# Kernel tuning notes

Measured on AMD Instinct MI355X. Metric: run time of the kernel, lower is better.

Reference implementation:

```python
import jax, jax.numpy as jnp
import numpy as np

FS, STRIDE, PAD = 3, 1, 1

def setup_inputs() -> dict:
    key = jax.random.key(0)
    k1, k2, k3 = jax.random.split(key, 3)
    N, C, H, W = 4, 256, 64, 64
    out_C = 256
    x = jax.random.normal(k1, (N, C, H, W), jnp.float32)
    # offset/mask conv params (original inits to 0 -> degenerate; use small random)
    offset_w = jax.random.normal(k2, (FS * FS * 3, C, FS, FS), jnp.float32) * 0.01
    offset_b = jnp.zeros((FS * FS * 3,), jnp.float32)
    # xavier_normal-like scale for dcn weight
    dcn_w = jax.random.normal(k3, (out_C, C, FS, FS), jnp.float32) * (1.0 / np.sqrt(C * FS * FS))
    return {"x": x, "offset_w": offset_w, "offset_b": offset_b, "dcn_w": dcn_w}

def _dcnv2(x, offset_w, offset_b, dcn_w):
    fs, stride, pad = FS, STRIDE, PAD
    N, C, H, W = x.shape
    out_C = dcn_w.shape[0]
    K2 = fs * fs
    om = jax.lax.conv_general_dilated(
        x, offset_w, (stride, stride), [(pad, pad), (pad, pad)],
        dimension_numbers=("NCHW", "OIHW", "NCHW")) + offset_b[None, :, None, None]
    Ho, Wo = om.shape[2], om.shape[3]
    offset = om[:, : 2 * K2].reshape(N, K2, 2, Ho, Wo)
    off_y, off_x = offset[:, :, 0], offset[:, :, 1]            # [N,K2,Ho,Wo]
    mask = jax.nn.sigmoid(om[:, 2 * K2:])                      # [N,K2,Ho,Wo]
    # base sampling grid: ori + kernel tap offset
    ky, kx = jnp.meshgrid(jnp.arange(fs), jnp.arange(fs), indexing="ij")
    ky = ky.reshape(K2).astype(jnp.float32)
    kx = kx.reshape(K2).astype(jnp.float32)
    base_y = (jnp.arange(Ho, dtype=jnp.float32) * stride - pad)[None, :, None] + ky[:, None, None]
    base_x = (jnp.arange(Wo, dtype=jnp.float32) * stride - pad)[None, None, :] + kx[:, None, None]
    h_im = base_y[None] + off_y                                # [N,K2,Ho,Wo]
    w_im = base_x[None] + off_x
    y0 = jnp.floor(h_im)
    x0 = jnp.floor(w_im)
    lh, lw = h_im - y0, w_im - x0
    xf = x.reshape(N, C, H * W)

    def gather(yi, xi):
        valid = (yi >= 0) & (yi <= H - 1) & (xi >= 0) & (xi <= W - 1)
        yc = jnp.clip(yi, 0, H - 1).astype(jnp.int32)
        xc = jnp.clip(xi, 0, W - 1).astype(jnp.int32)
        idx = (yc * W + xc).reshape(N, -1)
        v = jax.vmap(lambda img, ind: img[:, ind])(xf, idx)    # [N,C,K2*Ho*Wo]
        v = v.reshape(N, C, K2, Ho, Wo)
        return v * valid[:, None].astype(x.dtype)

    hh, hw = 1.0 - lh, 1.0 - lw
    sampled = ((hh * hw)[:, None] * gather(y0, x0)
               + (hh * lw)[:, None] * gather(y0, x0 + 1)
               + (lh * hw)[:, None] * gather(y0 + 1, x0)
               + (lh * lw)[:, None] * gather(y0 + 1, x0 + 1))  # [N,C,K2,Ho,Wo]
    sampled = sampled * mask[:, None]
    wk = dcn_w.reshape(out_C, C, K2)
    return jnp.einsum("nckhw,ock->nohw", sampled, wk)

def reference(x, offset_w, offset_b, dcn_w):
    return _dcnv2(x, offset_w, offset_b, dcn_w)
```

## Files before the change

### kernel.cpp

```cpp
#include <hip/hip_runtime.h>
#include <hip/hip_bf16.h>
#include <math.h>

#define NB     4
#define CIN    256
#define HH     64
#define WW     64
#define OUTC   256
#define K2     9
#define KTOT   2304
#define HWSZ   4096
#define NSTEPS 72
#define MTOT   16384


typedef __attribute__((ext_vector_type(4)))  float  floatx4;
typedef __attribute__((ext_vector_type(16))) float  floatx16;
typedef __attribute__((ext_vector_type(8)))  short  short8;
typedef __attribute__((ext_vector_type(4)))  short  short4v;
typedef __attribute__((ext_vector_type(4)))  int    intx4;

__device__ __forceinline__ unsigned short f2bf(float f) {
  union { float f; unsigned u; } v; v.f = f;
  unsigned r = v.u + 0x7FFF + ((v.u >> 16) & 1);
  return (unsigned short)(r >> 16);
}
__device__ __forceinline__ float b2f(unsigned short s) {
  union { unsigned u; float f; } v; v.u = ((unsigned)s) << 16;
  return v.f;
}

#define LDS_BARRIER() asm volatile("s_waitcnt lgkmcnt(0)\n\ts_barrier" ::: "memory")

#define WSM_BFRAG   0
#define WSM_B2FRAG  1179648
#define WSM_XT      (1179648 + 147456)
#define WSM_END     (WSM_XT + NB * HWSZ * CIN * 2)
#define WSF_BW      0
#define WSF_B2W     (KTOT * OUTC * 2)
#define WSF_OM      (WSF_B2W + KTOT * 32 * 2)
#define WSF_END     (WSF_OM + NB * 27 * HWSZ * 4)

__global__ __launch_bounds__(256) void prep_main_kernel(
    const float* __restrict__ dcn_w, const float* __restrict__ offw,
    const float* __restrict__ x,
    unsigned short* __restrict__ Bfrag, unsigned short* __restrict__ B2frag,
    unsigned short* __restrict__ xt) {
  int bid = blockIdx.x;
  int tid = threadIdx.x;
  if (bid < 256) {
    __shared__ unsigned short T[64 * 266];
    int img = bid >> 6, h = bid & 63;
    const float* xp = x + (size_t)img * CIN * HWSZ + h * 64;
    int w = tid & 63, cq = tid >> 6;
    for (int cb = 0; cb < 256; cb += 4) {
      int c = cb + cq;
      T[w * 266 + c] = f2bf(xp[(size_t)c * HWSZ + w]);
    }
    __syncthreads();
    int w2 = tid >> 2, cg = (tid & 3) << 6;
    unsigned short* o = xt + ((size_t)(img * 64 + h) * 64 + w2) * 256 + cg;
#pragma unroll
    for (int i = 0; i < 64; i += 8) {
      short8 v = *(short8*)&T[w2 * 266 + cg + i];
      *(short8*)(o + i) = v;
    }
  } else if (bid < 544) {
    int e = (bid - 256) * 256 + tid;
    int lane = e & 63, nt = (e >> 6) & 7, s16 = e >> 9;
    int n = nt * 32 + (lane & 31);
    int kb = s16 * 16 + ((lane >> 5) << 3);
    short8 pk;
#pragma unroll
    for (int j = 0; j < 8; ++j) {
      int k = kb + j;
      pk[j] = (short)f2bf(dcn_w[n * KTOT + (k & 255) * 9 + (k >> 8)]);
    }
    *(short8*)(Bfrag + (size_t)e * 8) = pk;
  } else {
    int e = (bid - 544) * 256 + tid;
    int lane = e & 63, nt = (e >> 6) & 1, s32 = e >> 7;
    int n = nt * 16 + (lane & 15);
    int kb = s32 * 32 + ((lane >> 4) << 3);
    short8 pk;
#pragma unroll
    for (int j = 0; j < 8; ++j) {
      int k = kb + j;
      pk[j] = (n < 27) ? (short)f2bf(offw[n * KTOT + (k & 255) * 9 + (k >> 8)])
                       : (short)0;
    }
    *(short8*)(B2frag + (size_t)e * 8) = pk;
  }
}

__global__ __launch_bounds__(512, 2) void dcn_fused_kernel(
    const unsigned short* __restrict__ xt,
    const unsigned short* __restrict__ Bfrag,
    const unsigned short* __restrict__ B2frag,
    const float* __restrict__ ob, float* __restrict__ out) {
  __shared__ unsigned short Ald[2][520 * 8];
  __shared__ intx4  sOff[576];
  __shared__ float4 sWt[576];
  __shared__ float  omp[4 * 32 * 68];

  int bid = blockIdx.x;
  int img = bid >> 6, h = bid & 63;
  const unsigned short* xb = xt + (size_t)img * HWSZ * 256;

  int tid  = threadIdx.x;
  int lane = tid & 63, q = tid >> 6;
  int quad = lane >> 4, l15 = lane & 15;
  int l31  = lane & 31,  lh5 = lane >> 5;

  if (q < 4) {
    floatx4 cacc[4][2];
#pragma unroll
    for (int mt = 0; mt < 4; ++mt)
#pragma unroll
      for (int nt = 0; nt < 2; ++nt) cacc[mt][nt] = (floatx4){0.f, 0.f, 0.f, 0.f};
    short8 cpa[2][4];
    short8 cpb[2][2];

#define CONV_LOAD(I, SLOT)                                                     \
  {                                                                            \
    int s = q + (I) * 4;                                                       \
    int t = s >> 3;                                                            \
    int dy = t / 3 - 1, dx = t % 3 - 1;                                        \
    int y = h + dy;                                                            \
    int cb0 = ((s & 7) << 5) + (quad << 3);                                    \
    _Pragma("unroll")                                                          \
    for (int mt = 0; mt < 4; ++mt) {                                           \
      int xx = mt * 16 + l15 + dx;                                             \
      short8 v = {0, 0, 0, 0, 0, 0, 0, 0};                                     \
      if (((unsigned)y < 64u) && ((unsigned)xx < 64u))                         \
        v = *(const short8*)(xb + ((y * 64 + xx) << 8) + cb0);                 \
      cpa[SLOT][mt] = v;                                                       \
    }                                                                          \
    _Pragma("unroll")                                                          \
    for (int nt = 0; nt < 2; ++nt)                                             \
      cpb[SLOT][nt] = *(const short8*)(B2frag + (((s * 2 + nt) * 64 + lane) << 3)); \
  }

    CONV_LOAD(0, 0);
#pragma unroll 2
    for (int i = 0; i < 18; ++i) {
      int sl = i & 1;
      if (i < 17) CONV_LOAD(i + 1, sl ^ 1);
#pragma unroll
      for (int mt = 0; mt < 4; ++mt)
#pragma unroll
        for (int nt = 0; nt < 2; ++nt)
          cacc[mt][nt] = __builtin_amdgcn_mfma_f32_16x16x32_bf16(
              cpa[sl][mt], cpb[sl][nt], cacc[mt][nt], 0, 0, 0);
    }
#undef CONV_LOAD
#pragma unroll
    for (int mt = 0; mt < 4; ++mt)
#pragma unroll
      for (int nt = 0; nt < 2; ++nt) {
        int oc = nt * 16 + l15;
        float4 vv = make_float4(cacc[mt][nt][0], cacc[mt][nt][1],
                                cacc[mt][nt][2], cacc[mt][nt][3]);
        *(float4*)&omp[(q * 32 + oc) * 68 + mt * 16 + quad * 4] = vv;
      }
  }
  __syncthreads();

  for (int v = tid; v < 576; v += 512) {
    int w = v & 63, t = v >> 6;
    int ky = t / 3, kx = t % 3;
    float offy = omp[(0 * 32 + 2 * t) * 68 + w] + omp[(1 * 32 + 2 * t) * 68 + w] +
                 omp[(2 * 32 + 2 * t) * 68 + w] + omp[(3 * 32 + 2 * t) * 68 + w] +
                 ob[2 * t];
    float offx = omp[(0 * 32 + 2 * t + 1) * 68 + w] + omp[(1 * 32 + 2 * t + 1) * 68 + w] +
                 omp[(2 * 32 + 2 * t + 1) * 68 + w] + omp[(3 * 32 + 2 * t + 1) * 68 + w] +
                 ob[2 * t + 1];
    float mraw = omp[(0 * 32 + 18 + t) * 68 + w] + omp[(1 * 32 + 18 + t) * 68 + w] +
                 omp[(2 * 32 + 18 + t) * 68 + w] + omp[(3 * 32 + 18 + t) * 68 + w] +
                 ob[18 + t];
    float mv   = 1.0f / (1.0f + __expf(-mraw));
    float him  = (float)(h - 1 + ky) + offy;
    float wim  = (float)(w - 1 + kx) + offx;
    float y0f = floorf(him), x0f = floorf(wim);
    float lhf = him - y0f, lwf = wim - x0f;
    int y0 = (int)y0f, x0i = (int)x0f;
    bool vy0 = (y0 >= 0) && (y0 < HH);
    bool vy1 = (y0 + 1 >= 0) && (y0 + 1 < HH);
    bool vx0 = (x0i >= 0) && (x0i < WW);
    bool vx1 = (x0i + 1 >= 0) && (x0i + 1 < WW);
    float hh_ = 1.0f - lhf, hw_ = 1.0f - lwf;
    float4 wt;
    wt.x = (vy0 && vx0) ? hh_ * hw_ * mv : 0.0f;
    wt.y = (vy0 && vx1) ? hh_ * lwf * mv : 0.0f;
    wt.z = (vy1 && vx0) ? lhf * hw_ * mv : 0.0f;
    wt.w = (vy1 && vx1) ? lhf * lwf * mv : 0.0f;
    int y0c = min(max(y0, 0), 63), y1c = min(max(y0 + 1, 0), 63);
    int x0c = min(max(x0i, 0), 63), x1c = min(max(x0i + 1, 0), 63);
    intx4 ii = {(y0c * 64 + x0c) << 8, (y0c * 64 + x1c) << 8,
                (y1c * 64 + x0c) << 8, (y1c * 64 + x1c) << 8};
    sOff[v] = ii;
    sWt[v]  = wt;
  }

  floatx16 acc[2];
#pragma unroll
  for (int mt = 0; mt < 2; ++mt)
#pragma unroll
    for (int e = 0; e < 16; ++e) acc[mt][e] = 0.f;

  int sm  = tid >> 3;
  int chk = tid & 7;
  int wgran = (((chk >> 1) << 1) + (sm >> 5)) * 65 + ((chk & 1) << 5) + (sm & 31);

  short8 bfr[2][4];
  short8 cr[4];
  float4 pwt;

  __syncthreads();

#pragma unroll
  for (int sub = 0; sub < 4; ++sub)
    bfr[0][sub] = *(const short8*)(
        Bfrag + (((size_t)sub * 8 + q) * 64 + lane) * 8);
  {
    intx4 off = sOff[sm];
    float4 w0 = sWt[sm];
    int cb = chk * 8;
    cr[0] = *(const short8*)(xb + off.x + cb);
    cr[1] = *(const short8*)(xb + off.y + cb);
    cr[2] = *(const short8*)(xb + off.z + cb);
    cr[3] = *(const short8*)(xb + off.w + cb);
    short8 pk;
#pragma unroll
    for (int j = 0; j < 8; ++j) {
      float v = w0.x * b2f((unsigned short)cr[0][j]) +
                w0.y * b2f((unsigned short)cr[1][j]) +
                w0.z * b2f((unsigned short)cr[2][j]) +
                w0.w * b2f((unsigned short)cr[3][j]);
      pk[j] = (short)f2bf(v);
    }
    *(short8*)&Ald[0][wgran * 8] = pk;
  }
  {
    intx4 off = sOff[sm];
    pwt = sWt[sm];
    int cb = 64 + chk * 8;
    cr[0] = *(const short8*)(xb + off.x + cb);
    cr[1] = *(const short8*)(xb + off.y + cb);
    cr[2] = *(const short8*)(xb + off.z + cb);
    cr[3] = *(const short8*)(xb + off.w + cb);
  }
  LDS_BARRIER();

#pragma unroll 2
  for (int s = 0; s < 36; ++s) {
    int cur = s & 1;
    if (s < 35) {
      int s16b = (s + 1) * 4;
#pragma unroll
      for (int sub = 0; sub < 4; ++sub)
        bfr[cur ^ 1][sub] = *(const short8*)(
            Bfrag + (((size_t)(s16b + sub) * 8 + q) * 64 + lane) * 8);
      short8 pk;
#pragma unroll
      for (int j = 0; j < 8; ++j) {
        float v = pwt.x * b2f((unsigned short)cr[0][j]) +
                  pwt.y * b2f((unsigned short)cr[1][j]) +
                  pwt.z * b2f((unsigned short)cr[2][j]) +
                  pwt.w * b2f((unsigned short)cr[3][j]);
        pk[j] = (short)f2bf(v);
      }
      *(short8*)&Ald[cur ^ 1][wgran * 8] = pk;
    }
    if (s < 34) {
      int s2 = s + 2;
      int t2 = s2 >> 2;
      intx4 off = sOff[t2 * 64 + sm];
      pwt = sWt[t2 * 64 + sm];
      int cb = (s2 & 3) * 64 + chk * 8;
      cr[0] = *(const short8*)(xb + off.x + cb);
      cr[1] = *(const short8*)(xb + off.y + cb);
      cr[2] = *(const short8*)(xb + off.z + cb);
      cr[3] = *(const short8*)(xb + off.w + cb);
    }
#pragma unroll
    for (int sub = 0; sub < 4; ++sub) {
      short8 a0 = *(short8*)&Ald[cur][((sub * 2 + 0) * 65 + lane) * 8];
      short8 a1 = *(short8*)&Ald[cur][((sub * 2 + 1) * 65 + lane) * 8];
      acc[0] = __builtin_amdgcn_mfma_f32_32x32x16_bf16(
          a0, bfr[cur][sub], acc[0], 0, 0, 0);
      acc[1] = __builtin_amdgcn_mfma_f32_32x32x16_bf16(
          a1, bfr[cur][sub], acc[1], 0, 0, 0);
    }
    LDS_BARRIER();
  }

  int oc = q * 32 + l31;
#pragma unroll
  for (int mt = 0; mt < 2; ++mt) {
    float* obase = out + (((size_t)img * OUTC + oc) << 12) + h * 64 +
                   mt * 32 + lh5 * 4;
#pragma unroll
    for (int rg = 0; rg < 4; ++rg) {
      float4 vv = make_float4(acc[mt][rg * 4 + 0], acc[mt][rg * 4 + 1],
                              acc[mt][rg * 4 + 2], acc[mt][rg * 4 + 3]);
      *(float4*)(obase + rg * 8) = vv;
    }
  }
}

__global__ __launch_bounds__(256) void prep_fb_kernel(
    const float* __restrict__ dcn_w, const float* __restrict__ offw,
    unsigned short* __restrict__ Bw, unsigned short* __restrict__ B2w) {
  int oc = blockIdx.x;
  for (int k = threadIdx.x; k < KTOT; k += 256) {
    int t = k >> 8, c = k & 255;
    Bw[oc * KTOT + k] = f2bf(dcn_w[oc * KTOT + c * 9 + t]);
    if (oc < 32)
      B2w[oc * KTOT + k] = (oc < 27) ? f2bf(offw[oc * KTOT + c * 9 + t])
                                     : (unsigned short)0;
  }
}

__global__ __launch_bounds__(256) void conv_offset_kernel(
    const float* __restrict__ x, const unsigned short* __restrict__ B2w,
    const float* __restrict__ ob, float* __restrict__ om) {
  __shared__ unsigned short A_lds[64 * 40];
  __shared__ unsigned short B_lds[32 * 40];
  int bid = blockIdx.x;
  int n = bid >> 6, h = bid & 63;
  int tid = threadIdx.x, lane = tid & 63, q = tid >> 6;
  const float* xn = x + n * (CIN * HWSZ);
  floatx4 acc0 = {0.f, 0.f, 0.f, 0.f}, acc1 = {0.f, 0.f, 0.f, 0.f};
  int w = tid & 63, cg = tid >> 6, ocb = tid >> 3, part = tid & 7;
  for (int s = 0; s < NSTEPS; ++s) {
    int t = s >> 3, c0 = (s & 7) << 5;
    int dy = t / 3 - 1, dx = t % 3 - 1;
    __syncthreads();
    {
      int y = h + dy, xx = w + dx;
      bool inb = ((unsigned)y < 64u) && ((unsigned)xx < 64u);
      const float* xb = xn + (c0 + cg * 8) * HWSZ + y * 64 + xx;
      short8 pk;
#pragma unroll
      for (int j = 0; j < 8; ++j) { float v = inb ? xb[j * HWSZ] : 0.0f; pk[j] = (short)f2bf(v); }
      *(short8*)&A_lds[w * 40 + cg * 8] = pk;
    }
    { const unsigned short* bp = B2w + ocb * KTOT + (t << 8) + c0 + part * 4;
      *(short4v*)&B_lds[ocb * 40 + part * 4] = *(const short4v*)bp; }
    __syncthreads();
    int fr = (lane >> 4) * 8;
    short8 af  = *(short8*)&A_lds[(q * 16 + (lane & 15)) * 40 + fr];
    short8 bf0 = *(short8*)&B_lds[((lane & 15)) * 40 + fr];
    short8 bf1 = *(short8*)&B_lds[(16 + (lane & 15)) * 40 + fr];
    acc0 = __builtin_amdgcn_mfma_f32_16x16x32_bf16(af, bf0, acc0, 0, 0, 0);
    acc1 = __builtin_amdgcn_mfma_f32_16x16x32_bf16(af, bf1, acc1, 0, 0, 0);
  }
  int g = lane >> 4;
#pragma unroll
  for (int nt = 0; nt < 2; ++nt) {
    floatx4 a = nt ? acc1 : acc0;
    int oc = nt * 16 + (lane & 15);
    if (oc < 27) {
      float bias = ob[oc];
#pragma unroll
      for (int r = 0; r < 4; ++r) {
        int wm = q * 16 + g * 4 + r;
        float val = a[r] + bias;
        if (oc >= 18) val = 1.0f / (1.0f + __expf(-val));
        om[((n * 27 + oc) << 12) + h * 64 + wm] = val;
      }
    }
  }
}

__global__ __launch_bounds__(256) void dcn_main_kernel(
    const float* __restrict__ x, const float* __restrict__ om,
    const unsigned short* __restrict__ Bw, float* __restrict__ out) {
  __shared__ unsigned short A_lds[32 * 40];
  __shared__ unsigned short B_lds[256 * 40];
  __shared__ int    sY[288];
  __shared__ int    sX[288];
  __shared__ float4 sW[288];
  int bid = blockIdx.x;
  int n = bid >> 7, rem = bid & 127, h = rem >> 1, w0 = (rem & 1) << 5;
  int tid = threadIdx.x, lane = tid & 63, q = tid >> 6;
  const float* xn  = x + n * (CIN * HWSZ);
  const float* omn = om + n * (27 * HWSZ);
  for (int v = tid; v < 288; v += 256) {
    int m = v & 31, t = v >> 5;
    int ky = t / 3, kx = t % 3;
    int wg = w0 + m, sp = h * 64 + wg;
    float offy = omn[(2 * t) * HWSZ + sp];
    float offx = omn[(2 * t + 1) * HWSZ + sp];
    float mv   = omn[(18 + t) * HWSZ + sp];
    float him = (float)(h - 1 + ky) + offy;
    float wim = (float)(wg - 1 + kx) + offx;
    float y0f = floorf(him), x0f = floorf(wim);
    float lh = him - y0f, lw = wim - x0f;
    int y0 = (int)y0f, x0i = (int)x0f;
    bool vy0 = (y0 >= 0) && (y0 < HH), vy1 = (y0 + 1 >= 0) && (y0 + 1 < HH);
    bool vx0 = (x0i >= 0) && (x0i < WW), vx1 = (x0i + 1 >= 0) && (x0i + 1 < WW);
    float hh_ = 1.0f - lh, hw_ = 1.0f - lw;
    float4 wt;
    wt.x = (vy0 && vx0) ? hh_ * hw_ * mv : 0.0f;
    wt.y = (vy0 && vx1) ? hh_ * lw  * mv : 0.0f;
    wt.z = (vy1 && vx0) ? lh  * hw_ * mv : 0.0f;
    wt.w = (vy1 && vx1) ? lh  * lw  * mv : 0.0f;
    sY[v] = y0; sX[v] = x0i; sW[v] = wt;
  }
  floatx4 acc[2][4];
#pragma unroll
  for (int mi = 0; mi < 2; ++mi)
#pragma unroll
    for (int nj = 0; nj < 4; ++nj) acc[mi][nj] = (floatx4){0.f, 0.f, 0.f, 0.f};
  int m = tid & 31, cg = tid >> 5, n0 = q * 64;
  for (int s = 0; s < NSTEPS; ++s) {
    int t = s >> 3, c0 = (s & 7) << 5;
    __syncthreads();
    {
      int p = t * 32 + m;
      int y0 = sY[p], x0i = sX[p];
      float4 wt = sW[p];
      int y0c = min(max(y0, 0), 63), y1c = min(max(y0 + 1, 0), 63);
      int x0c = min(max(x0i, 0), 63), x1c = min(max(x0i + 1, 0), 63);
      int i00 = y0c * 64 + x0c, i01 = y0c * 64 + x1c;
      int i10 = y1c * 64 + x0c, i11 = y1c * 64 + x1c;
      const float* xb = xn + (c0 + cg * 4) * HWSZ;
      short4v pk;
#pragma unroll
      for (int j = 0; j < 4; ++j) {
        const float* xc = xb + j * HWSZ;
        float v = wt.x * xc[i00] + wt.y * xc[i01] + wt.z * xc[i10] + wt.w * xc[i11];
        pk[j] = (short)f2bf(v);
      }
      *(short4v*)&A_lds[m * 40 + cg * 4] = pk;
    }
    {
      const short8* bp = (const short8*)(Bw + tid * KTOT + (t << 8) + c0);
      short8 b0 = bp[0], b1 = bp[1], b2 = bp[2], b3 = bp[3];
      short8* dst = (short8*)&B_lds[tid * 40];
      dst[0] = b0; dst[1] = b1; dst[2] = b2; dst[3] = b3;
    }
    __syncthreads();
    int fr = (lane >> 4) * 8;
    short8 a0 = *(short8*)&A_lds[((lane & 15)) * 40 + fr];
    short8 a1 = *(short8*)&A_lds[(16 + (lane & 15)) * 40 + fr];
#pragma unroll
    for (int nj = 0; nj < 4; ++nj) {
      short8 bfp = *(short8*)&B_lds[(n0 + nj * 16 + (lane & 15)) * 40 + fr];
      acc[0][nj] = __builtin_amdgcn_mfma_f32_16x16x32_bf16(a0, bfp, acc[0][nj], 0, 0, 0);
      acc[1][nj] = __builtin_amdgcn_mfma_f32_16x16x32_bf16(a1, bfp, acc[1][nj], 0, 0, 0);
    }
  }
  int g = lane >> 4;
#pragma unroll
  for (int mi = 0; mi < 2; ++mi) {
    int wm = w0 + mi * 16 + g * 4;
#pragma unroll
    for (int nj = 0; nj < 4; ++nj) {
      int oc = n0 + nj * 16 + (lane & 15);
      float4 vv = make_float4(acc[mi][nj][0], acc[mi][nj][1],
                              acc[mi][nj][2], acc[mi][nj][3]);
      *(float4*)&out[((n * OUTC + oc) << 12) + h * 64 + wm] = vv;
    }
  }
}

extern "C" void kernel_launch(void* const* d_in, const int* in_sizes, int n_in,
                              void* d_out, int out_size, void* d_ws, size_t ws_size,
                              hipStream_t stream) {
  const float* x     = (const float*)d_in[0];
  const float* offw  = (const float*)d_in[1];
  const float* ob    = (const float*)d_in[2];
  const float* dcn_w = (const float*)d_in[3];
  float* out = (float*)d_out;

  if (ws_size >= (size_t)WSM_END) {
    unsigned short* Bfrag  = (unsigned short*)((char*)d_ws + WSM_BFRAG);
    unsigned short* B2frag = (unsigned short*)((char*)d_ws + WSM_B2FRAG);
    unsigned short* xtb    = (unsigned short*)((char*)d_ws + WSM_XT);
    prep_main_kernel<<<580, 256, 0, stream>>>(dcn_w, offw, x, Bfrag, B2frag, xtb);
    dcn_fused_kernel<<<256, 512, 0, stream>>>(xtb, Bfrag, B2frag, ob, out);
  } else {
    unsigned short* Bw  = (unsigned short*)((char*)d_ws + WSF_BW);
    unsigned short* B2w = (unsigned short*)((char*)d_ws + WSF_B2W);
    float*          omb = (float*)((char*)d_ws + WSF_OM);
    prep_fb_kernel<<<256, 256, 0, stream>>>(dcn_w, offw, Bw, B2w);
    conv_offset_kernel<<<NB * HH, 256, 0, stream>>>(x, B2w, ob, omb);
    dcn_main_kernel<<<NB * HH * 2, 256, 0, stream>>>(x, omb, Bw, out);
  }
}
```

Measured before the change: 126.3 us.

## Deepen sampling pipeline, stage weight repack through LDS, packed bf16 convert, block swizzle

The main loop now uses four LDS A-buffers with bilinear samples prefetched two steps ahead. MFMA sections are wrapped in s_setprio to favour matrix issue. Bilinear blending now uses packed int loads and the hardware v_cvt_pk_bf16_f32 instruction instead of a manual round-to-bf16. The weight-repacking prep blocks read rows of dcn_w/offw into LDS with coalesced loads rather than strided global gathers, which cuts the prep grid from 580 to 328 blocks. Block IDs are also remapped across images. Together these aim to hide gather latency and trim prep-kernel cost, at the price of more registers and LDS, which may reduce occupancy.

```diff
diff --git a/kernel.cpp b/kernel.cpp
--- a/kernel.cpp
+++ b/kernel.cpp
@@ -28,6 +28,32 @@
 __device__ __forceinline__ float b2f(unsigned short s) {
   union { unsigned u; float f; } v; v.u = ((unsigned)s) << 16;
   return v.f;
+}
+__device__ __forceinline__ float lo16f(int u) {
+  union { int i; float f; } v; v.i = u << 16; return v.f;
+}
+__device__ __forceinline__ float hi16f(int u) {
+  union { int i; float f; } v; v.i = u & 0xFFFF0000; return v.f;
+}
+__device__ __forceinline__ unsigned cvt_pk_bf16(float lo, float hi) {
+  unsigned r;
+  asm("v_cvt_pk_bf16_f32 %0, %1, %2" : "=v"(r) : "v"(lo), "v"(hi));
+  return r;
+}
+
+__device__ __forceinline__ void pack8(const intx4& c0, const intx4& c1,
+                                      const intx4& c2, const intx4& c3,
+                                      const float4& w, unsigned short* dst) {
+  intx4 o;
+#pragma unroll
+  for (int jj = 0; jj < 4; ++jj) {
+    float v0 = w.x * lo16f(c0[jj]) + w.y * lo16f(c1[jj]) +
+               w.z * lo16f(c2[jj]) + w.w * lo16f(c3[jj]);
+    float v1 = w.x * hi16f(c0[jj]) + w.y * hi16f(c1[jj]) +
+               w.z * hi16f(c2[jj]) + w.w * hi16f(c3[jj]);
+    o[jj] = (int)cvt_pk_bf16(v0, v1);
+  }
+  *(intx4*)dst = o;
 }
 
 #define LDS_BARRIER() asm volatile("s_waitcnt lgkmcnt(0)\n\ts_barrier" ::: "memory")
@@ -65,31 +91,53 @@
       short8 v = *(short8*)&T[w2 * 266 + cg + i];
       *(short8*)(o + i) = v;
     }
-  } else if (bid < 544) {
-    int e = (bid - 256) * 256 + tid;
-    int lane = e & 63, nt = (e >> 6) & 7, s16 = e >> 9;
-    int n = nt * 32 + (lane & 31);
-    int kb = s16 * 16 + ((lane >> 5) << 3);
-    short8 pk;
-#pragma unroll
-    for (int j = 0; j < 8; ++j) {
-      int k = kb + j;
-      pk[j] = (short)f2bf(dcn_w[n * KTOT + (k & 255) * 9 + (k >> 8)]);
-    }
-    *(short8*)(Bfrag + (size_t)e * 8) = pk;
+  } else if (bid < 320) {
+    __shared__ unsigned short W[4 * KTOT];
+    int n0 = (bid - 256) * 4;
+#pragma unroll
+    for (int r = 0; r < 4; ++r)
+      for (int c = tid; c < KTOT; c += 256)
+        W[r * KTOT + c] = f2bf(dcn_w[(size_t)(n0 + r) * KTOT + c]);
+    __syncthreads();
+    for (int i = tid; i < 1152; i += 256) {
+      int s16 = i >> 3, hf = (i >> 2) & 1, nl = i & 3;
+      int n = n0 + nl;
+      int lane = (hf << 5) + (n & 31);
+      int e = (((s16 << 3) + (n >> 5)) << 6) + lane;
+      int kb = (s16 << 4) + (hf << 3);
+      short8 pk;
+#pragma unroll
+      for (int j = 0; j < 8; ++j) {
+        int k = kb + j;
+        pk[j] = (short)W[nl * KTOT + (k & 255) * 9 + (k >> 8)];
+      }
+      *(short8*)(Bfrag + (size_t)e * 8) = pk;
+    }
   } else {
-    int e = (bid - 544) * 256 + tid;
-    int lane = e & 63, nt = (e >> 6) & 1, s32 = e >> 7;
-    int n = nt * 16 + (lane & 15);
-    int kb = s32 * 32 + ((lane >> 4) << 3);
-    short8 pk;
-#pragma unroll
-    for (int j = 0; j < 8; ++j) {
-      int k = kb + j;
-      pk[j] = (n < 27) ? (short)f2bf(offw[n * KTOT + (k & 255) * 9 + (k >> 8)])
-                       : (short)0;
-    }
-    *(short8*)(B2frag + (size_t)e * 8) = pk;
+    __shared__ unsigned short W2[4 * KTOT];
+    int n0 = (bid - 320) * 4;
+#pragma unroll
+    for (int r = 0; r < 4; ++r) {
+      bool ok = (n0 + r) < 27;
+      for (int c = tid; c < KTOT; c += 256)
+        W2[r * KTOT + c] = ok ? f2bf(offw[(size_t)(n0 + r) * KTOT + c])
+                              : (unsigned short)0;
+    }
+    __syncthreads();
+    for (int i = tid; i < 1152; i += 256) {
+      int s32 = i >> 4, qq = (i >> 2) & 3, nl = i & 3;
+      int n = n0 + nl;
+      int lane = (qq << 4) + (n & 15);
+      int e = (((s32 << 1) + (n >> 4)) << 6) + lane;
+      int kb = (s32 << 5) + (qq << 3);
+      short8 pk;
+#pragma unroll
+      for (int j = 0; j < 8; ++j) {
+        int k = kb + j;
+        pk[j] = (short)W2[nl * KTOT + (k & 255) * 9 + (k >> 8)];
+      }
+      *(short8*)(B2frag + (size_t)e * 8) = pk;
+    }
   }
 }
 
@@ -98,12 +146,13 @@
     const unsigned short* __restrict__ Bfrag,
     const unsigned short* __restrict__ B2frag,
     const float* __restrict__ ob, float* __restrict__ out) {
-  __shared__ unsigned short Ald[2][520 * 8];
+  __shared__ unsigned short Ald[4][520 * 8];
   __shared__ intx4  sOff[576];
   __shared__ float4 sWt[576];
   __shared__ float  omp[4 * 32 * 68];
 
-  int bid = blockIdx.x;
+  int braw = blockIdx.x;
+  int bid  = ((braw & 7) << 5) + (braw >> 3);
   int img = bid >> 6, h = bid & 63;
   const unsigned short* xb = xt + (size_t)img * HWSZ * 256;
 
@@ -213,84 +262,118 @@
   int wgran = (((chk >> 1) << 1) + (sm >> 5)) * 65 + ((chk & 1) << 5) + (sm & 31);
 
   short8 bfr[2][4];
-  short8 cr[4];
-  float4 pwt;
+  intx4  cr[2][4];
+  float4 pwt[2];
 
   __syncthreads();
 
 #pragma unroll
-  for (int sub = 0; sub < 4; ++sub)
+  for (int sub = 0; sub < 4; ++sub) {
     bfr[0][sub] = *(const short8*)(
-        Bfrag + (((size_t)sub * 8 + q) * 64 + lane) * 8);
+        Bfrag + (((size_t)(0 + sub) * 8 + q) * 64 + lane) * 8);
+    bfr[1][sub] = *(const short8*)(
+        Bfrag + (((size_t)(4 + sub) * 8 + q) * 64 + lane) * 8);
+  }
   {
     intx4 off = sOff[sm];
     float4 w0 = sWt[sm];
-    int cb = chk * 8;
-    cr[0] = *(const short8*)(xb + off.x + cb);
-    cr[1] = *(const short8*)(xb + off.y + cb);
-    cr[2] = *(const short8*)(xb + off.z + cb);
-    cr[3] = *(const short8*)(xb + off.w + cb);
-    short8 pk;
-#pragma unroll
-    for (int j = 0; j < 8; ++j) {
-      float v = w0.x * b2f((unsigned short)cr[0][j]) +
-                w0.y * b2f((unsigned short)cr[1][j]) +
-                w0.z * b2f((unsigned short)cr[2][j]) +
-                w0.w * b2f((unsigned short)cr[3][j]);
-      pk[j] = (short)f2bf(v);
-    }
-    *(short8*)&Ald[0][wgran * 8] = pk;
-  }
-  {
-    intx4 off = sOff[sm];
-    pwt = sWt[sm];
-    int cb = 64 + chk * 8;
-    cr[0] = *(const short8*)(xb + off.x + cb);
-    cr[1] = *(const short8*)(xb + off.y + cb);
-    cr[2] = *(const short8*)(xb + off.z + cb);
-    cr[3] = *(const short8*)(xb + off.w + cb);
+    {
+      int cb = chk * 8;
+      intx4 c0 = *(const intx4*)(xb + off.x + cb);
+      intx4 c1 = *(const intx4*)(xb + off.y + cb);
+      intx4 c2 = *(const intx4*)(xb + off.z + cb);
+      intx4 c3 = *(const intx4*)(xb + off.w + cb);
+      pack8(c0, c1, c2, c3, w0, &Ald[0][wgran * 8]);
+    }
+    {
+      int cb = 64 + chk * 8;
+      intx4 c0 = *(const intx4*)(xb + off.x + cb);
+      intx4 c1 = *(const intx4*)(xb + off.y + cb);
+      intx4 c2 = *(const intx4*)(xb + off.z + cb);
+      intx4 c3 = *(const intx4*)(xb + off.w + cb);
+      pack8(c0, c1, c2, c3, w0, &Ald[1][wgran * 8]);
+    }
+    {
+      int cb = 128 + chk * 8;
+      pwt[0] = w0;
+      cr[0][0] = *(const intx4*)(xb + off.x + cb);
+      cr[0][1] = *(const intx4*)(xb + off.y + cb);
+      cr[0][2] = *(const intx4*)(xb + off.z + cb);
+      cr[0][3] = *(const intx4*)(xb + off.w + cb);
+    }
+    {
+      int cb = 192 + chk * 8;
+      pwt[1] = w0;
+      cr[1][0] = *(const intx4*)(xb + off.x + cb);
+      cr[1][1] = *(const intx4*)(xb + off.y + cb);
+      cr[1][2] = *(const intx4*)(xb + off.z + cb);
+      cr[1][3] = *(const intx4*)(xb + off.w + cb);
+    }
   }
   LDS_BARRIER();
 
 #pragma unroll 2
-  for (int s = 0; s < 36; ++s) {
-    int cur = s & 1;
-    if (s < 35) {
-      int s16b = (s + 1) * 4;
+  for (int S = 0; S < 18; ++S) {
+    int s0 = 2 * S, s1 = s0 + 1;
+    __builtin_amdgcn_s_setprio(1);
+#pragma unroll
+    for (int sub = 0; sub < 4; ++sub) {
+      short8 a0 = *(short8*)&Ald[s0 & 3][((sub * 2 + 0) * 65 + lane) * 8];
+      short8 a1 = *(short8*)&Ald[s0 & 3][((sub * 2 + 1) * 65 + lane) * 8];
+      acc[0] = __builtin_amdgcn_mfma_f32_32x32x16_bf16(
+          a0, bfr[0][sub], acc[0], 0, 0, 0);
+      acc[1] = __builtin_amdgcn_mfma_f32_32x32x16_bf16(
+          a1, bfr[0][sub], acc[1], 0, 0, 0);
+    }
+    __builtin_amdgcn_s_setprio(0);
+    if (s0 + 2 < 36) {
+      int s16b = (s0 + 2) * 4;
 #pragma unroll
       for (int sub = 0; sub < 4; ++sub)
-        bfr[cur ^ 1][sub] = *(const short8*)(
+        bfr[0][sub] = *(const short8*)(
             Bfrag + (((size_t)(s16b + sub) * 8 + q) * 64 + lane) * 8);
-      short8 pk;
-#pragma unroll
-      for (int j = 0; j < 8; ++j) {
-        float v = pwt.x * b2f((unsigned short)cr[0][j]) +
-                  pwt.y * b2f((unsigned short)cr[1][j]) +
-                  pwt.z * b2f((unsigned short)cr[2][j]) +
-                  pwt.w * b2f((unsigned short)cr[3][j]);
-        pk[j] = (short)f2bf(v);
-      }
-      *(short8*)&Ald[cur ^ 1][wgran * 8] = pk;
-    }
-    if (s < 34) {
-      int s2 = s + 2;
-      int t2 = s2 >> 2;
-      intx4 off = sOff[t2 * 64 + sm];
-      pwt = sWt[t2 * 64 + sm];
-      int cb = (s2 & 3) * 64 + chk * 8;
-      cr[0] = *(const short8*)(xb + off.x + cb);
-      cr[1] = *(const short8*)(xb + off.y + cb);
-      cr[2] = *(const short8*)(xb + off.z + cb);
-      cr[3] = *(const short8*)(xb + off.w + cb);
-    }
+      pack8(cr[0][0], cr[0][1], cr[0][2], cr[0][3], pwt[0],
+            &Ald[(s0 + 2) & 3][wgran * 8]);
+    }
+    if (s0 + 4 < 36) {
+      int s4 = s0 + 4, t4 = s4 >> 2;
+      intx4 off = sOff[t4 * 64 + sm];
+      pwt[0] = sWt[t4 * 64 + sm];
+      int cb = (s4 & 3) * 64 + chk * 8;
+      cr[0][0] = *(const intx4*)(xb + off.x + cb);
+      cr[0][1] = *(const intx4*)(xb + off.y + cb);
+      cr[0][2] = *(const intx4*)(xb + off.z + cb);
+      cr[0][3] = *(const intx4*)(xb + off.w + cb);
+    }
+    __builtin_amdgcn_s_setprio(1);
 #pragma unroll
     for (int sub = 0; sub < 4; ++sub) {
-      short8 a0 = *(short8*)&Ald[cur][((sub * 2 + 0) * 65 + lane) * 8];
-      short8 a1 = *(short8*)&Ald[cur][((sub * 2 + 1) * 65 + lane) * 8];
+      short8 a0 = *(short8*)&Ald[s1 & 3][((sub * 2 + 0) * 65 + lane) * 8];
+      short8 a1 = *(short8*)&Ald[s1 & 3][((sub * 2 + 1) * 65 + lane) * 8];
       acc[0] = __builtin_amdgcn_mfma_f32_32x32x16_bf16(
-          a0, bfr[cur][sub], acc[0], 0, 0, 0);
+          a0, bfr[1][sub], acc[0], 0, 0, 0);
       acc[1] = __builtin_amdgcn_mfma_f32_32x32x16_bf16(
-          a1, bfr[cur][sub], acc[1], 0, 0, 0);
+          a1, bfr[1][sub], acc[1], 0, 0, 0);
+    }
+    __builtin_amdgcn_s_setprio(0);
+    if (s1 + 2 < 36) {
+      int s16b = (s1 + 2) * 4;
+#pragma unroll
+      for (int sub = 0; sub < 4; ++sub)
+        bfr[1][sub] = *(const short8*)(
+            Bfrag + (((size_t)(s16b + sub) * 8 + q) * 64 + lane) * 8);
+      pack8(cr[1][0], cr[1][1], cr[1][2], cr[1][3], pwt[1],
+            &Ald[(s1 + 2) & 3][wgran * 8]);
+    }
+    if (s1 + 4 < 36) {
+      int s4 = s1 + 4, t4 = s4 >> 2;
+      intx4 off = sOff[t4 * 64 + sm];
+      pwt[1] = sWt[t4 * 64 + sm];
+      int cb = (s4 & 3) * 64 + chk * 8;
+      cr[1][0] = *(const intx4*)(xb + off.x + cb);
+      cr[1][1] = *(const intx4*)(xb + off.y + cb);
+      cr[1][2] = *(const intx4*)(xb + off.z + cb);
+      cr[1][3] = *(const intx4*)(xb + off.w + cb);
     }
     LDS_BARRIER();
   }
@@ -480,7 +563,7 @@
     unsigned short* Bfrag  = (unsigned short*)((char*)d_ws + WSM_BFRAG);
     unsigned short* B2frag = (unsigned short*)((char*)d_ws + WSM_B2FRAG);
     unsigned short* xtb    = (unsigned short*)((char*)d_ws + WSM_XT);
-    prep_main_kernel<<<580, 256, 0, stream>>>(dcn_w, offw, x, Bfrag, B2frag, xtb);
+    prep_main_kernel<<<328, 256, 0, stream>>>(dcn_w, offw, x, Bfrag, B2frag, xtb);
     dcn_fused_kernel<<<256, 512, 0, stream>>>(xtb, Bfrag, B2frag, ob, out);
   } else {
     unsigned short* Bw  = (unsigned short*)((char*)d_ws + WSF_BW);
```

Result: slower. 130.7 us (+3.5%).
